# Optimization experiments

Measured on AMD Instinct MI355X. Metric: run time of the kernel, lower is better.

The kernel has to match this reference:

```python
import jax, jax.numpy as jnp
import numpy as np

NEG_INF = -1e30  # stands in for torch's -inf diagonal mask; exp() underflows to 0 identically


def conv1x1(x, w, b):
    # x: [B,C,H,W], w: [O,C], b: [O]
    return jnp.einsum('oc,bchw->bohw', w, x) + b[None, :, None, None]


def s_module(x, qw, qb, kw, kb, vw, vb, gamma):
    # CCNet criss-cross attention with -inf diagonal masking on the H branch.
    B, C, H, W = x.shape
    q = conv1x1(x, qw, qb)  # [B,C8,H,W]
    k = conv1x1(x, kw, kb)  # [B,C8,H,W]
    v = conv1x1(x, vw, vb)  # [B,C,H,W]
    # energy_H[b,h,w,g] = <q[b,:,h,w], k[b,:,g,w]>  (attend along column)
    e_h = jnp.einsum('bchw,bcgw->bhwg', q, k)
    diag_mask = jnp.where(jnp.eye(H, dtype=bool), NEG_INF, 0.0).astype(x.dtype)
    e_h = e_h + diag_mask[None, :, None, :]  # mask h == g
    # energy_W[b,h,w,v] = <q[b,:,h,w], k[b,:,h,v]>  (attend along row)
    e_w = jnp.einsum('bchw,bchv->bhwv', q, k)
    att = jax.nn.softmax(jnp.concatenate([e_h, e_w], axis=-1), axis=-1)  # [B,H,W,H+W]
    a_h, a_w = att[..., :H], att[..., H:]
    out_h = jnp.einsum('bcgw,bhwg->bchw', v, a_h)
    out_w = jnp.einsum('bchv,bhwv->bchw', v, a_w)
    return gamma * (out_h + out_w) + x


def cam_module(x, fb, gamma):
    # channel attention: energy [B,C,C], max-sub trick, softmax, bmm back
    B, C, H, W = x.shape
    f = fb.reshape(B, C, H * W)
    energy = jnp.einsum('bcn,bdn->bcd', f, f)
    energy_new = jnp.max(energy, axis=-1, keepdims=True) - energy
    att = jax.nn.softmax(energy_new, axis=-1)
    out = jnp.einsum('bcd,bdn->bcn', att, f).reshape(B, C, H, W)
    return x + gamma * out


def _forward(x, fb, w_conv, b_conv, bn_g, bn_b,
             xq_w, xq_b, xk_w, xk_b, xv_w, xv_b, x_gamma,
             fq_w, fq_b, fk_w, fk_b, fv_w, fv_b, f_gamma,
             pam_gamma, pam_gamma2, cam_gamma):
    # MaxPool2d(kernel=2, stride=2)
    fbd = jax.lax.reduce_window(fb, -jnp.inf, jax.lax.max,
                                (1, 1, 2, 2), (1, 1, 2, 2), 'VALID')
    # convblock: 1x1 conv + BatchNorm (training-mode batch stats) + ReLU
    y = conv1x1(fbd, w_conv, b_conv)
    mu = jnp.mean(y, axis=(0, 2, 3), keepdims=True)
    var = jnp.var(y, axis=(0, 2, 3), keepdims=True)
    y = (y - mu) * jax.lax.rsqrt(var + 1e-5)
    y = y * bn_g[None, :, None, None] + bn_b[None, :, None, None]
    y = jax.nn.relu(y)
    # FeedbackSpatialAttention (PAM)
    x_att = pam_gamma * s_module(x, xq_w, xq_b, xk_w, xk_b, xv_w, xv_b, x_gamma)
    fb_att = s_module(y, fq_w, fq_b, fk_w, fk_b, fv_w, fv_b, f_gamma)
    pam_out = x + x_att + pam_gamma2 * fb_att
    # CAM on (x, processed fb)
    cam_out = cam_module(x, y, cam_gamma)
    return pam_out + cam_out


def setup_inputs() -> dict:
    key = jax.random.key(0)
    ks = jax.random.split(key, 24)
    B, C, H, W = 4, 64, 128, 128
    C8 = C // 8
    d = {
        'x': jax.random.normal(ks[0], (B, C, H, W), jnp.float32),
        'fb': jax.random.normal(ks[1], (B, C, 2 * H, 2 * W), jnp.float32),
        'w_conv': jax.random.normal(ks[2], (C, C), jnp.float32) * 0.05,
        'b_conv': jax.random.normal(ks[3], (C,), jnp.float32) * 0.02,
        'bn_g': jax.random.uniform(ks[4], (C,), jnp.float32, 0.5, 1.5),
        'bn_b': jax.random.normal(ks[5], (C,), jnp.float32) * 0.02,
        'xq_w': jax.random.normal(ks[6], (C8, C), jnp.float32) * 0.05,
        'xq_b': jax.random.normal(ks[7], (C8,), jnp.float32) * 0.02,
        'xk_w': jax.random.normal(ks[8], (C8, C), jnp.float32) * 0.05,
        'xk_b': jax.random.normal(ks[9], (C8,), jnp.float32) * 0.02,
        'xv_w': jax.random.normal(ks[10], (C, C), jnp.float32) * 0.05,
        'xv_b': jax.random.normal(ks[11], (C,), jnp.float32) * 0.02,
        'x_gamma': jax.random.normal(ks[12], (1,), jnp.float32) * 0.1,
        'fq_w': jax.random.normal(ks[13], (C8, C), jnp.float32) * 0.05,
        'fq_b': jax.random.normal(ks[14], (C8,), jnp.float32) * 0.02,
        'fk_w': jax.random.normal(ks[15], (C8, C), jnp.float32) * 0.05,
        'fk_b': jax.random.normal(ks[16], (C8,), jnp.float32) * 0.02,
        'fv_w': jax.random.normal(ks[17], (C, C), jnp.float32) * 0.05,
        'fv_b': jax.random.normal(ks[18], (C,), jnp.float32) * 0.02,
        'f_gamma': jax.random.normal(ks[19], (1,), jnp.float32) * 0.1,
        'pam_gamma': jax.random.normal(ks[20], (1,), jnp.float32) * 0.1,
        'pam_gamma2': jax.random.normal(ks[21], (1,), jnp.float32) * 0.1,
        'cam_gamma': jax.random.normal(ks[22], (1,), jnp.float32) * 0.1,
    }
    return d


def reference(x, fb, w_conv, b_conv, bn_g, bn_b,
              xq_w, xq_b, xk_w, xk_b, xv_w, xv_b, x_gamma,
              fq_w, fq_b, fk_w, fk_b, fv_w, fv_b, f_gamma,
              pam_gamma, pam_gamma2, cam_gamma):
    return _forward(x, fb, w_conv, b_conv, bn_g, bn_b,
                    xq_w, xq_b, xk_w, xk_b, xv_w, xv_b, x_gamma,
                    fq_w, fq_b, fk_w, fk_b, fv_w, fv_b, f_gamma,
                    pam_gamma, pam_gamma2, cam_gamma)
```

## Files before the change

### kernel.cpp

```cpp
#include <hip/hip_runtime.h>
#include <hip/hip_bf16.h>

#define NP 16384
#define NB 4

typedef __hip_bfloat16 bf16;
typedef unsigned short u16;
typedef unsigned short us8 __attribute__((ext_vector_type(8)));
typedef short ss8 __attribute__((ext_vector_type(8)));
typedef float f32x4 __attribute__((ext_vector_type(4)));
__device__ __forceinline__ float bf2f(const bf16 v) { return __bfloat162float(v); }
__device__ __forceinline__ bf16 f2bf(float v) { return __float2bfloat16(v); }
__device__ __forceinline__ float bfu(u16 h) {
  return __uint_as_float(((unsigned)h) << 16);
}
__device__ __forceinline__ u16 fbu(float v) {
  bf16 b = f2bf(v);
  return *(u16*)&b;
}


__global__ __launch_bounds__(256) void k_pool_conv(
    const float* __restrict__ fb, const float* __restrict__ wconv,
    const float* __restrict__ bconv, bf16* __restrict__ Y) {
  __shared__ float wS[64 * 65], bS[64], Xs[4096];
  int tid = threadIdx.x;
  int b = blockIdx.x >> 8, tile = blockIdx.x & 255;
  int n0 = tile * 64;
  for (int i = tid; i < 4096; i += 256) wS[(i >> 6) * 65 + (i & 63)] = wconv[i];
  if (tid < 64) bS[tid] = bconv[tid];
  for (int i = tid; i < 4096; i += 256) {
    int c = i >> 6, px = i & 63;
    int n = n0 + px, h = n >> 7, w = n & 127;
    size_t fbase = ((size_t)((b * 64 + c) * 256 + 2 * h)) * 256 + 2 * w;
    float2 v01 = *(const float2*)(fb + fbase);
    float2 v23 = *(const float2*)(fb + fbase + 256);
    Xs[i] = fmaxf(fmaxf(v01.x, v01.y), fmaxf(v23.x, v23.y));
  }
  __syncthreads();
  int ty = tid >> 4, tx = tid & 15;
  float acc[4][4];
#pragma unroll
  for (int i = 0; i < 4; ++i) {
    float bv = bS[ty + 16 * i];
#pragma unroll
    for (int j = 0; j < 4; ++j) acc[i][j] = bv;
  }
  for (int c = 0; c < 64; ++c) {
    float xv[4], wv[4];
#pragma unroll
    for (int j = 0; j < 4; ++j) xv[j] = Xs[c * 64 + tx * 4 + j];
#pragma unroll
    for (int i = 0; i < 4; ++i) wv[i] = wS[(ty + 16 * i) * 65 + c];
#pragma unroll
    for (int i = 0; i < 4; ++i)
#pragma unroll
      for (int j = 0; j < 4; ++j) acc[i][j] = fmaf(wv[i], xv[j], acc[i][j]);
  }
#pragma unroll
  for (int i = 0; i < 4; ++i) {
    int ch = ty + 16 * i;
    bf16* yb = Y + (size_t)(b * 64 + ch) * NP + n0 + tx * 4;
#pragma unroll
    for (int j = 0; j < 4; ++j) yb[j] = f2bf(acc[i][j]);
  }
}

__global__ __launch_bounds__(256) void k_stats_p1(const bf16* __restrict__ Y,
                                                  float* __restrict__ PS) {
  int blk = blockIdx.x, tid = threadIdx.x;
  int o = blk >> 3, slab = blk & 7;
  int b = slab >> 1, half = slab & 1;
  const us8* vp =
      (const us8*)(Y + ((size_t)(b * 64 + o)) * NP + half * 8192);
  float s = 0.f, ss = 0.f;
#pragma unroll
  for (int it = 0; it < 4; ++it) {
    us8 v = vp[tid + 256 * it];
#pragma unroll
    for (int e = 0; e < 8; ++e) {
      float f = bfu(v[e]);
      s += f;
      ss = fmaf(f, f, ss);
    }
  }
  for (int off = 32; off > 0; off >>= 1) {
    s += __shfl_down(s, off, 64);
    ss += __shfl_down(ss, off, 64);
  }
  __shared__ float sh[8];
  int wv = tid >> 6, ln = tid & 63;
  if (ln == 0) { sh[wv] = s; sh[4 + wv] = ss; }
  __syncthreads();
  if (tid == 0) {
    PS[blk] = sh[0] + sh[1] + sh[2] + sh[3];
    PS[512 + blk] = sh[4] + sh[5] + sh[6] + sh[7];
  }
}

__global__ __launch_bounds__(64) void k_stats_p2(
    const float* __restrict__ PS, const float* __restrict__ bng,
    const float* __restrict__ bnb, float* __restrict__ SCALE,
    float* __restrict__ SHIFT, const float* xg, const float* fg,
    const float* pg, const float* pg2, const float* cg,
    float* __restrict__ HDR) {
  int o = threadIdx.x;
  float s = 0.f, ss = 0.f;
#pragma unroll
  for (int k = 0; k < 8; ++k) {
    s += PS[o * 8 + k];
    ss += PS[512 + o * 8 + k];
  }
  const float inv = 1.0f / (NB * NP);
  float mu = s * inv;
  float var = ss * inv - mu * mu;
  float r = rsqrtf(var + 1e-5f);
  float sc = r * bng[o];
  SCALE[o] = sc;
  SHIFT[o] = bnb[o] - mu * sc;
  if (o == 0) {
    float vpg = pg[0];
    HDR[1] = vpg * xg[0];
    HDR[2] = pg2[0] * fg[0];
    HDR[3] = 2.0f + vpg;
    HDR[4] = pg2[0];
    HDR[5] = cg[0];
  }
}

__global__ __launch_bounds__(256) void k_conv80x2(
    const float* __restrict__ xin, const bf16* __restrict__ Yin,
    const float* __restrict__ SCALE, const float* __restrict__ SHIFT,
    const float* __restrict__ qw0, const float* __restrict__ qb0,
    const float* __restrict__ kw0, const float* __restrict__ kb0,
    const float* __restrict__ vw0, const float* __restrict__ vb0,
    const float* __restrict__ qw1, const float* __restrict__ qb1,
    const float* __restrict__ kw1, const float* __restrict__ kb1,
    const float* __restrict__ vw1, const float* __restrict__ vb1,
    bf16* __restrict__ QK, bf16* __restrict__ V) {
  __shared__ float wS[80 * 65], bS[80];
  __shared__ u16 Xs[4096];
  int tid = threadIdx.x;
  int m = blockIdx.x >> 10;
  int rest = blockIdx.x & 1023;
  int b = rest >> 8, tile = rest & 255;
  int n0 = tile * 64;
  const float* qw = m ? qw1 : qw0;
  const float* qb = m ? qb1 : qb0;
  const float* kw = m ? kw1 : kw0;
  const float* kb = m ? kb1 : kb0;
  const float* vw = m ? vw1 : vw0;
  const float* vb = m ? vb1 : vb0;
  for (int i = tid; i < 512; i += 256) {
    wS[(i >> 6) * 65 + (i & 63)] = qw[i];
    wS[(8 + (i >> 6)) * 65 + (i & 63)] = kw[i];
  }
  for (int i = tid; i < 4096; i += 256)
    wS[(16 + (i >> 6)) * 65 + (i & 63)] = vw[i];
  if (tid < 8) { bS[tid] = qb[tid]; bS[8 + tid] = kb[tid]; }
  if (tid < 64) bS[16 + tid] = vb[tid];
  for (int i = tid; i < 4096; i += 256) {
    int c = i >> 6, px = i & 63;
    size_t idx = (size_t)(b * 64 + c) * NP + n0 + px;
    float v;
    if (m) {
      v = bf2f(Yin[idx]);
      v = fmaf(v, SCALE[c], SHIFT[c]);
      v = fmaxf(v, 0.f);
    } else {
      v = xin[idx];
    }
    Xs[i] = fbu(v);
  }
  __syncthreads();
  int ty = tid >> 4, tx = tid & 15;
  float acc[5][4];
#pragma unroll
  for (int i = 0; i < 5; ++i) {
    float bv = bS[ty + 16 * i];
#pragma unroll
    for (int j = 0; j < 4; ++j) acc[i][j] = bv;
  }
  for (int c = 0; c < 64; ++c) {
    float xv[4], wv[5];
#pragma unroll
    for (int j = 0; j < 4; ++j) xv[j] = bfu(Xs[c * 64 + tx * 4 + j]);
#pragma unroll
    for (int i = 0; i < 5; ++i) wv[i] = wS[(ty + 16 * i) * 65 + c];
#pragma unroll
    for (int i = 0; i < 5; ++i)
#pragma unroll
      for (int j = 0; j < 4; ++j) acc[i][j] = fmaf(wv[i], xv[j], acc[i][j]);
  }
#pragma unroll
  for (int i = 0; i < 5; ++i) {
    int ch = ty + 16 * i;
    bf16* dst;
    size_t base;
    if (ch < 8) {
      dst = QK; base = (size_t)(((m * 2 + 0) * 4 + b) * 8 + ch) * NP;
    } else if (ch < 16) {
      dst = QK; base = (size_t)(((m * 2 + 1) * 4 + b) * 8 + (ch - 8)) * NP;
    } else {
      dst = V; base = (size_t)((m * 4 + b) * 64 + (ch - 16)) * NP;
    }
#pragma unroll
    for (int j = 0; j < 4; ++j) dst[base + n0 + tx * 4 + j] = f2bf(acc[i][j]);
  }
}

__global__ __launch_bounds__(256) void k_transpose2(
    const u16* __restrict__ inA, u16* __restrict__ outA,
    const u16* __restrict__ inB, u16* __restrict__ outB, int nA) {
  int tileId = blockIdx.x & 15;
  int plane = blockIdx.x >> 4;
  const u16* ip;
  u16* op;
  if (plane < nA) {
    ip = inA + (size_t)plane * NP;
    op = outA + (size_t)plane * NP;
  } else {
    ip = inB + (size_t)(plane - nA) * NP;
    op = outB + (size_t)(plane - nA) * NP;
  }
  int th = tileId >> 2, tw = tileId & 3;
  __shared__ u16 t[32][33];
  int lx = threadIdx.x & 31, ly = threadIdx.x >> 5;
  for (int i = 0; i < 32; i += 8)
    t[ly + i][lx] = ip[(size_t)(th * 32 + ly + i) * 128 + tw * 32 + lx];
  __syncthreads();
  for (int i = 0; i < 32; i += 8)
    op[(size_t)(tw * 32 + ly + i) * 128 + th * 32 + lx] = t[lx][ly + i];
}

__global__ __launch_bounds__(256) void k_qk_stats(
    const bf16* __restrict__ QK, const bf16* __restrict__ QKT,
    float* __restrict__ MW, float* __restrict__ LW,
    float* __restrict__ MH, float* __restrict__ LH) {
  int blk = blockIdx.x;
  int m = blk & 1, mode = (blk >> 1) & 1;
  int bid = blk >> 2;
  int b = bid >> 7, pl = bid & 127;
  const bf16* basep = mode ? QKT : QK;
  const bf16* Qp = basep + (size_t)(((m * 2 + 0) * 4 + b) * 8) * NP;
  const bf16* Kp = basep + (size_t)(((m * 2 + 1) * 4 + b) * 8) * NP;
  float* Mo = (mode ? MH : MW) + (size_t)(m * 4 + b) * NP;
  float* Lo = (mode ? LH : LW) + (size_t)(m * 4 + b) * NP;
  __shared__ float qs[1024], ks[1024], red[256];
  int tid = threadIdx.x;
  for (int i = tid; i < 1024; i += 256) {
    int c = i >> 7, j = i & 127;
    qs[i] = bf2f(Qp[(size_t)c * NP + (size_t)pl * 128 + j]);
    ks[i] = bf2f(Kp[(size_t)c * NP + (size_t)pl * 128 + j]);
  }
  __syncthreads();
  int w = tid & 127, half = tid >> 7;
  float qr[8];
#pragma unroll
  for (int c = 0; c < 8; ++c) qr[c] = qs[c * 128 + w];
  float scr[64];
  float mx = -3.0e38f;
#pragma unroll
  for (int v0 = 0; v0 < 64; ++v0) {
    int v = half * 64 + v0;
    float s = 0.f;
#pragma unroll
    for (int c = 0; c < 8; ++c) s = fmaf(qr[c], ks[c * 128 + v], s);
    if (mode && v == w) s = -1.0e30f;
    scr[v0] = s;
    mx = fmaxf(mx, s);
  }
  red[tid] = mx;
  __syncthreads();
  float mj = fmaxf(red[w], red[128 + w]);
  __syncthreads();
  float l = 0.f;
#pragma unroll
  for (int v0 = 0; v0 < 64; ++v0) l += __expf(scr[v0] - mj);
  red[tid] = l;
  __syncthreads();
  if (half == 0) {
    Mo[(size_t)pl * 128 + w] = mj;
    Lo[(size_t)pl * 128 + w] = red[w] + red[128 + w];
  }
}

__global__ __launch_bounds__(256, 4) void k_av(
    const bf16* __restrict__ QK, const bf16* __restrict__ QKT,
    const bf16* __restrict__ V, const bf16* __restrict__ VT,
    const float* __restrict__ MW, const float* __restrict__ LW,
    const float* __restrict__ MH, const float* __restrict__ LH,
    float* __restrict__ OW, bf16* __restrict__ OHT) {
  int blk = blockIdx.x;
  int m = blk & 1, mode = (blk >> 1) & 1;
  int bid = blk >> 2;
  int b = bid >> 7, h = bid & 127;
  const bf16* qkbase = mode ? QKT : QK;
  const bf16* Qp = qkbase + (size_t)(((m * 2 + 0) * 4 + b) * 8) * NP;
  const bf16* Kp = qkbase + (size_t)(((m * 2 + 1) * 4 + b) * 8) * NP;
  const bf16* Vp = (mode ? VT : V) + (size_t)((m * 4 + b) * 64) * NP;
  __shared__ __align__(16) u16 qT[128 * 8];
  __shared__ __align__(16) u16 kT[128 * 8];
  __shared__ __align__(16) u16 Vs[64 * 136];
  __shared__ float Ml[128], Li[128];
  int tid = threadIdx.x;
  {
    int c = (tid >> 4) & 7, vj = tid & 15;
    const bf16* src = (tid < 128) ? Qp : Kp;
    u16* dst = (tid < 128) ? qT : kT;
    const us8* sp = (const us8*)(src + (size_t)c * NP + (size_t)h * 128);
    us8 sv = sp[vj];
#pragma unroll
    for (int e = 0; e < 8; ++e) {
      int j = vj * 8 + e;
      int p = ((j & 7) << 4) | (j >> 3);
      dst[p * 8 + c] = sv[e];
    }
  }
  for (int i2 = tid; i2 < 1024; i2 += 256) {
    int c = i2 >> 4, vj = i2 & 15;
    const us8* vp = (const us8*)(Vp + (size_t)c * NP + (size_t)h * 128);
    us8 vv = vp[vj];
    *(us8*)&Vs[c * 136 + vj * 8] = vv;
  }
  if (tid < 128) {
    size_t sb = (size_t)(m * 4 + b) * NP;
    const float* Mc = mode ? MH : MW;
    const float* Lc = mode ? LH : LW;
    const float* Ms = mode ? MW : MH;
    const float* Ls = mode ? LW : LH;
    float mc = Mc[sb + (size_t)h * 128 + tid];
    float lc = Lc[sb + (size_t)h * 128 + tid];
    float ms = Ms[sb + (size_t)tid * 128 + h];
    float ls = Ls[sb + (size_t)tid * 128 + h];
    float mm = fmaxf(mc, ms);
    float ll = lc * __expf(mc - mm) + ls * __expf(ms - mm);
    Ml[tid] = mm;
    Li[tid] = 1.0f / ll;
  }
  __syncthreads();
  int lane = tid & 63, wv = tid >> 6;
  int il = lane & 15, gq = lane >> 4;
  float* owBase = OW + (size_t)((m * 4 + b) * 64) * NP + (size_t)h * 128;
  bf16* ohBase = OHT + (size_t)((m * 4 + b) * 64) * NP + (size_t)h * 128;
#pragma unroll
  for (int sub = 0; sub < 2; ++sub) {
    int ib = wv * 32 + sub * 16;
    int i = ib + il;
    float mv = Ml[i], li = Li[i];
    int pi = ((i & 7) << 4) | (i >> 3);
    us8 qv = *(const us8*)&qT[pi * 8];
    float qr[8];
#pragma unroll
    for (int c = 0; c < 8; ++c) qr[c] = bfu(qv[c]);
    ss8 afr[4];
#pragma unroll
    for (int ks = 0; ks < 4; ++ks) {
      ss8 af;
#pragma unroll
      for (int e = 0; e < 8; ++e) {
        int j = ks * 32 + gq * 8 + e;
        int pj = ((j & 7) << 4) | (j >> 3);
        us8 kv = *(const us8*)&kT[pj * 8];
        float s = 0.f;
#pragma unroll
        for (int c = 0; c < 8; ++c) s = fmaf(qr[c], bfu(kv[c]), s);
        float ev = __expf(s - mv) * li;
        if (mode && j == i) ev = 0.f;
        af[e] = (short)fbu(ev);
      }
      afr[ks] = af;
    }
#pragma unroll
    for (int ct = 0; ct < 4; ++ct) {
      f32x4 acc = {0.f, 0.f, 0.f, 0.f};
#pragma unroll
      for (int ks = 0; ks < 4; ++ks) {
        ss8 bv = *(const ss8*)&Vs[(ct * 16 + il) * 136 + ks * 32 + gq * 8];
        acc = __builtin_amdgcn_mfma_f32_16x16x32_bf16(afr[ks], bv, acc, 0, 0, 0);
      }
      int cch = ct * 16 + il;
      int i0 = ib + gq * 4;
      if (mode == 0) {
#pragma unroll
        for (int r = 0; r < 4; ++r)
          owBase[(size_t)cch * NP + (size_t)(i0 + r)] = acc[r];
      } else {
#pragma unroll
        for (int r = 0; r < 4; ++r)
          ohBase[(size_t)cch * NP + (size_t)(i0 + r)] = f2bf(acc[r]);
      }
    }
  }
}

__global__ __launch_bounds__(256) void k_merge2(const bf16* __restrict__ OHT,
                                                float* __restrict__ ACC,
                                                const float* __restrict__ HDR) {
  int tileId = blockIdx.x & 15;
  int plane = blockIdx.x >> 4;
  int th = tileId >> 2, tw = tileId & 3;
  __shared__ float t0[32][33], t1[32][33];
  int lx = threadIdx.x & 31, ly = threadIdx.x >> 5;
  const bf16* ip0 = OHT + (size_t)plane * NP;
  const bf16* ip1 = OHT + (size_t)(256 + plane) * NP;
  for (int i = 0; i < 32; i += 8) {
    size_t idx = (size_t)(th * 32 + ly + i) * 128 + tw * 32 + lx;
    t0[ly + i][lx] = bf2f(ip0[idx]);
    t1[ly + i][lx] = bf2f(ip1[idx]);
  }
  __syncthreads();
  float sc0 = HDR[1], sc1 = HDR[2];
  float* op = ACC + (size_t)plane * NP;
  for (int i = 0; i < 32; i += 8) {
    int h = tw * 32 + ly + i, w = th * 32 + lx;
    op[(size_t)h * 128 + w] = sc0 * t0[lx][ly + i] + sc1 * t1[lx][ly + i];
  }
}

__global__ __launch_bounds__(256) void k_gram(const bf16* __restrict__ Y,
                                              const float* __restrict__ SCALE,
                                              const float* __restrict__ SHIFT,
                                              float* __restrict__ GP) {
  int b = blockIdx.x >> 7, ch = (blockIdx.x >> 2) & 31, t = blockIdx.x & 3;
  int tid = threadIdx.x;
  __shared__ float fs[64 * 129];
  int cg = tid >> 4, dg = tid & 15;
  float acc[4][4];
#pragma unroll
  for (int i = 0; i < 4; ++i)
#pragma unroll
    for (int jx = 0; jx < 4; ++jx) acc[i][jx] = 0.f;
  const bf16* yb = Y + (size_t)b * 64 * NP + ch * 512;
  for (int idx = tid; idx < 8192; idx += 256) {
    int c = idx >> 7, j = idx & 127;
    float v = fmaf(bf2f(yb[(size_t)c * NP + t * 128 + j]), SCALE[c], SHIFT[c]);
    fs[c * 129 + j] = fmaxf(v, 0.f);
  }
  __syncthreads();
  for (int j = 0; j < 128; ++j) {
    float a[4], d[4];
#pragma unroll
    for (int i = 0; i < 4; ++i) a[i] = fs[(cg * 4 + i) * 129 + j];
#pragma unroll
    for (int i = 0; i < 4; ++i) d[i] = fs[(dg * 4 + i) * 129 + j];
#pragma unroll
    for (int i = 0; i < 4; ++i)
#pragma unroll
      for (int jx = 0; jx < 4; ++jx) acc[i][jx] = fmaf(a[i], d[jx], acc[i][jx]);
  }
  float* gp = GP + ((size_t)(b * 128) + ch * 4 + t) * 4096;
#pragma unroll
  for (int i = 0; i < 4; ++i)
#pragma unroll
    for (int jx = 0; jx < 4; ++jx)
      gp[(cg * 4 + i) * 64 + dg * 4 + jx] = acc[i][jx];
}

__global__ __launch_bounds__(256) void k_gram_reduce(const float* __restrict__ GP,
                                                     float* __restrict__ CATT) {
  int b = blockIdx.x >> 4, rg = blockIdx.x & 15;
  int tid = threadIdx.x;
  __shared__ float Es[256];
  int e = rg * 256 + tid;
  float s = 0.f;
  for (int k = 0; k < 128; ++k) s += GP[((size_t)b * 128 + k) * 4096 + e];
  Es[tid] = s;
  __syncthreads();
  int wv = tid >> 6, ln = tid & 63;
  float v = Es[wv * 64 + ln];
  float mn = v;
  for (int off = 32; off; off >>= 1) mn = fminf(mn, __shfl_xor(mn, off, 64));
  float ev = __expf(mn - v);
  float ssum = ev;
  for (int off = 32; off; off >>= 1) ssum += __shfl_xor(ssum, off, 64);
  CATT[((size_t)b * 64 + rg * 4 + wv) * 64 + ln] = ev / ssum;
}

__global__ __launch_bounds__(256) void k_final(
    const float* __restrict__ x, const bf16* __restrict__ Y,
    const float* __restrict__ SCALE, const float* __restrict__ SHIFT,
    const float* __restrict__ CATT, const float* __restrict__ OW,
    const float* __restrict__ HDR, float* __restrict__ OUT) {
  __shared__ float attS[64 * 65], Ys[64 * 65];
  int tid = threadIdx.x;
  int b = blockIdx.x >> 8, tile = blockIdx.x & 255;
  int n0 = tile * 64;
  for (int i = tid; i < 4096; i += 256)
    attS[(i >> 6) * 65 + (i & 63)] = CATT[(size_t)b * 4096 + i];
  for (int i = tid; i < 4096; i += 256) {
    int d = i >> 6, px = i & 63;
    float v = fmaf(bf2f(Y[(size_t)(b * 64 + d) * NP + n0 + px]), SCALE[d], SHIFT[d]);
    Ys[d * 65 + px] = fmaxf(v, 0.f);
  }
  __syncthreads();
  int cg = tid >> 4, pgx = tid & 15;
  int c0 = cg * 4, p0 = pgx * 4;
  float acc[4][4];
#pragma unroll
  for (int i = 0; i < 4; ++i)
#pragma unroll
    for (int j = 0; j < 4; ++j) acc[i][j] = 0.f;
  for (int d = 0; d < 64; ++d) {
    float a[4], yv[4];
#pragma unroll
    for (int i = 0; i < 4; ++i) a[i] = attS[(c0 + i) * 65 + d];
#pragma unroll
    for (int j = 0; j < 4; ++j) yv[j] = Ys[d * 65 + p0 + j];
#pragma unroll
    for (int i = 0; i < 4; ++i)
#pragma unroll
      for (int j = 0; j < 4; ++j) acc[i][j] = fmaf(a[i], yv[j], acc[i][j]);
  }
  float c2pg = HDR[3], fpg2 = HDR[4], fcg = HDR[5];
  float sc0 = HDR[1], sc1 = HDR[2];
#pragma unroll
  for (int i = 0; i < 4; ++i) {
    size_t base = (size_t)(b * 64 + c0 + i) * NP + n0 + p0;
    const float* ow0 = OW + base;
    const float* ow1 = OW + (size_t)256 * NP + base;
#pragma unroll
    for (int j = 0; j < 4; ++j) {
      float yv = Ys[(c0 + i) * 65 + p0 + j];
      OUT[base + j] = c2pg * x[base + j] + fpg2 * yv + OUT[base + j] +
                      fcg * acc[i][j] + sc0 * ow0[j] + sc1 * ow1[j];
    }
  }
}

extern "C" void kernel_launch(void* const* d_in, const int* in_sizes, int n_in,
                              void* d_out, int out_size, void* d_ws, size_t ws_size,
                              hipStream_t stream) {
  const float* x = (const float*)d_in[0];
  const float* fbp = (const float*)d_in[1];

  char* base = (char*)d_ws;
  float* HDR = (float*)base;
  float* SCALE = HDR + 16;
  float* SHIFT = SCALE + 64;
  char* p = base + 4096;
  bf16* Y = (bf16*)p;    p += 8388608;
  bf16* QK = (bf16*)p;   p += 4194304;
  bf16* QKT = (bf16*)p;  p += 4194304;
  bf16* V = (bf16*)p;    p += 16777216;
  bf16* VT = (bf16*)p;   p += 16777216;
  float* MW = (float*)p; p += 524288;
  float* LW = (float*)p; p += 524288;
  float* MH = (float*)p; p += 524288;
  float* LH = (float*)p; p += 524288;
  bf16* OHT = (bf16*)p;  p += 16777216;
  float* OW = (float*)p; p += 33554432;
  float* GP = (float*)p; p += 8388608;
  float* CATT = (float*)p; p += 1048576;
  float* ACC = (float*)d_out;
  float* PS = (float*)QK;

  k_pool_conv<<<1024, 256, 0, stream>>>(fbp, (const float*)d_in[2],
                                        (const float*)d_in[3], Y);
  k_stats_p1<<<512, 256, 0, stream>>>(Y, PS);
  k_stats_p2<<<1, 64, 0, stream>>>(PS, (const float*)d_in[4],
                                   (const float*)d_in[5], SCALE, SHIFT,
                                   (const float*)d_in[12], (const float*)d_in[19],
                                   (const float*)d_in[20], (const float*)d_in[21],
                                   (const float*)d_in[22], HDR);

  k_conv80x2<<<2048, 256, 0, stream>>>(
      x, Y, SCALE, SHIFT,
      (const float*)d_in[6], (const float*)d_in[7], (const float*)d_in[8],
      (const float*)d_in[9], (const float*)d_in[10], (const float*)d_in[11],
      (const float*)d_in[13], (const float*)d_in[14], (const float*)d_in[15],
      (const float*)d_in[16], (const float*)d_in[17], (const float*)d_in[18],
      QK, V);
  k_transpose2<<<10240, 256, 0, stream>>>((const u16*)QK, (u16*)QKT,
                                          (const u16*)V, (u16*)VT, 128);
  k_qk_stats<<<2048, 256, 0, stream>>>(QK, QKT, MW, LW, MH, LH);
  k_av<<<2048, 256, 0, stream>>>(QK, QKT, V, VT, MW, LW, MH, LH, OW, OHT);
  k_merge2<<<4096, 256, 0, stream>>>(OHT, ACC, HDR);

  k_gram<<<512, 256, 0, stream>>>(Y, SCALE, SHIFT, GP);
  k_gram_reduce<<<64, 256, 0, stream>>>(GP, CATT);
  k_final<<<1024, 256, 0, stream>>>(x, Y, SCALE, SHIFT, CATT, OW, HDR,
                                    (float*)d_out);
}
```

Baseline: 311.6 us.

## Fuse softmax stats into attention kernel and merge partial outputs flash-style

```diff
diff --git a/kernel.cpp b/kernel.cpp
--- a/kernel.cpp
+++ b/kernel.cpp
@@ -233,63 +233,11 @@
     op[(size_t)(tw * 32 + ly + i) * 128 + th * 32 + lx] = t[lx][ly + i];
 }
 
-__global__ __launch_bounds__(256) void k_qk_stats(
-    const bf16* __restrict__ QK, const bf16* __restrict__ QKT,
-    float* __restrict__ MW, float* __restrict__ LW,
-    float* __restrict__ MH, float* __restrict__ LH) {
-  int blk = blockIdx.x;
-  int m = blk & 1, mode = (blk >> 1) & 1;
-  int bid = blk >> 2;
-  int b = bid >> 7, pl = bid & 127;
-  const bf16* basep = mode ? QKT : QK;
-  const bf16* Qp = basep + (size_t)(((m * 2 + 0) * 4 + b) * 8) * NP;
-  const bf16* Kp = basep + (size_t)(((m * 2 + 1) * 4 + b) * 8) * NP;
-  float* Mo = (mode ? MH : MW) + (size_t)(m * 4 + b) * NP;
-  float* Lo = (mode ? LH : LW) + (size_t)(m * 4 + b) * NP;
-  __shared__ float qs[1024], ks[1024], red[256];
-  int tid = threadIdx.x;
-  for (int i = tid; i < 1024; i += 256) {
-    int c = i >> 7, j = i & 127;
-    qs[i] = bf2f(Qp[(size_t)c * NP + (size_t)pl * 128 + j]);
-    ks[i] = bf2f(Kp[(size_t)c * NP + (size_t)pl * 128 + j]);
-  }
-  __syncthreads();
-  int w = tid & 127, half = tid >> 7;
-  float qr[8];
-#pragma unroll
-  for (int c = 0; c < 8; ++c) qr[c] = qs[c * 128 + w];
-  float scr[64];
-  float mx = -3.0e38f;
-#pragma unroll
-  for (int v0 = 0; v0 < 64; ++v0) {
-    int v = half * 64 + v0;
-    float s = 0.f;
-#pragma unroll
-    for (int c = 0; c < 8; ++c) s = fmaf(qr[c], ks[c * 128 + v], s);
-    if (mode && v == w) s = -1.0e30f;
-    scr[v0] = s;
-    mx = fmaxf(mx, s);
-  }
-  red[tid] = mx;
-  __syncthreads();
-  float mj = fmaxf(red[w], red[128 + w]);
-  __syncthreads();
-  float l = 0.f;
-#pragma unroll
-  for (int v0 = 0; v0 < 64; ++v0) l += __expf(scr[v0] - mj);
-  red[tid] = l;
-  __syncthreads();
-  if (half == 0) {
-    Mo[(size_t)pl * 128 + w] = mj;
-    Lo[(size_t)pl * 128 + w] = red[w] + red[128 + w];
-  }
-}
-
 __global__ __launch_bounds__(256, 4) void k_av(
     const bf16* __restrict__ QK, const bf16* __restrict__ QKT,
     const bf16* __restrict__ V, const bf16* __restrict__ VT,
-    const float* __restrict__ MW, const float* __restrict__ LW,
-    const float* __restrict__ MH, const float* __restrict__ LH,
+    float* __restrict__ MWp, float* __restrict__ LWp,
+    float* __restrict__ MHp, float* __restrict__ LHp,
     float* __restrict__ OW, bf16* __restrict__ OHT) {
   int blk = blockIdx.x;
   int m = blk & 1, mode = (blk >> 1) & 1;
@@ -302,7 +250,6 @@
   __shared__ __align__(16) u16 qT[128 * 8];
   __shared__ __align__(16) u16 kT[128 * 8];
   __shared__ __align__(16) u16 Vs[64 * 136];
-  __shared__ float Ml[128], Li[128];
   int tid = threadIdx.x;
   {
     int c = (tid >> 4) & 7, vj = tid & 15;
@@ -323,40 +270,25 @@
     us8 vv = vp[vj];
     *(us8*)&Vs[c * 136 + vj * 8] = vv;
   }
-  if (tid < 128) {
-    size_t sb = (size_t)(m * 4 + b) * NP;
-    const float* Mc = mode ? MH : MW;
-    const float* Lc = mode ? LH : LW;
-    const float* Ms = mode ? MW : MH;
-    const float* Ls = mode ? LW : LH;
-    float mc = Mc[sb + (size_t)h * 128 + tid];
-    float lc = Lc[sb + (size_t)h * 128 + tid];
-    float ms = Ms[sb + (size_t)tid * 128 + h];
-    float ls = Ls[sb + (size_t)tid * 128 + h];
-    float mm = fmaxf(mc, ms);
-    float ll = lc * __expf(mc - mm) + ls * __expf(ms - mm);
-    Ml[tid] = mm;
-    Li[tid] = 1.0f / ll;
-  }
   __syncthreads();
   int lane = tid & 63, wv = tid >> 6;
   int il = lane & 15, gq = lane >> 4;
+  size_t sb = (size_t)(m * 4 + b) * NP;
   float* owBase = OW + (size_t)((m * 4 + b) * 64) * NP + (size_t)h * 128;
   bf16* ohBase = OHT + (size_t)((m * 4 + b) * 64) * NP + (size_t)h * 128;
 #pragma unroll
   for (int sub = 0; sub < 2; ++sub) {
     int ib = wv * 32 + sub * 16;
     int i = ib + il;
-    float mv = Ml[i], li = Li[i];
     int pi = ((i & 7) << 4) | (i >> 3);
     us8 qv = *(const us8*)&qT[pi * 8];
     float qr[8];
 #pragma unroll
     for (int c = 0; c < 8; ++c) qr[c] = bfu(qv[c]);
-    ss8 afr[4];
+    float scr[4][8];
+    float mrow = -3.0e38f;
 #pragma unroll
     for (int ks = 0; ks < 4; ++ks) {
-      ss8 af;
 #pragma unroll
       for (int e = 0; e < 8; ++e) {
         int j = ks * 32 + gq * 8 + e;
@@ -365,11 +297,36 @@
         float s = 0.f;
 #pragma unroll
         for (int c = 0; c < 8; ++c) s = fmaf(qr[c], bfu(kv[c]), s);
-        float ev = __expf(s - mv) * li;
-        if (mode && j == i) ev = 0.f;
+        if (mode && j == i) s = -1.0e30f;
+        scr[ks][e] = s;
+        mrow = fmaxf(mrow, s);
+      }
+    }
+    mrow = fmaxf(mrow, __shfl_xor(mrow, 16, 64));
+    mrow = fmaxf(mrow, __shfl_xor(mrow, 32, 64));
+    float l = 0.f;
+    ss8 afr[4];
+#pragma unroll
+    for (int ks = 0; ks < 4; ++ks) {
+      ss8 af;
+#pragma unroll
+      for (int e = 0; e < 8; ++e) {
+        float ev = __expf(scr[ks][e] - mrow);
+        l += ev;
         af[e] = (short)fbu(ev);
       }
       afr[ks] = af;
+    }
+    l += __shfl_xor(l, 16, 64);
+    l += __shfl_xor(l, 32, 64);
+    if (gq == 0) {
+      if (mode == 0) {
+        MWp[sb + (size_t)h * 128 + i] = mrow;
+        LWp[sb + (size_t)h * 128 + i] = l;
+      } else {
+        MHp[sb + (size_t)i * 128 + h] = mrow;
+        LHp[sb + (size_t)i * 128 + h] = l;
+      }
     }
 #pragma unroll
     for (int ct = 0; ct < 4; ++ct) {
@@ -394,11 +351,14 @@
   }
 }
 
-__global__ __launch_bounds__(256) void k_merge2(const bf16* __restrict__ OHT,
-                                                float* __restrict__ ACC,
-                                                const float* __restrict__ HDR) {
+__global__ __launch_bounds__(256) void k_merge2(
+    const bf16* __restrict__ OHT, const float* __restrict__ OW,
+    const float* __restrict__ MWp, const float* __restrict__ LWp,
+    const float* __restrict__ MHp, const float* __restrict__ LHp,
+    const float* __restrict__ HDR, float* __restrict__ ACC) {
   int tileId = blockIdx.x & 15;
   int plane = blockIdx.x >> 4;
+  int b = plane >> 6;
   int th = tileId >> 2, tw = tileId & 3;
   __shared__ float t0[32][33], t1[32][33];
   int lx = threadIdx.x & 31, ly = threadIdx.x >> 5;
@@ -412,9 +372,23 @@
   __syncthreads();
   float sc0 = HDR[1], sc1 = HDR[2];
   float* op = ACC + (size_t)plane * NP;
+  const float* ow0 = OW + (size_t)plane * NP;
+  const float* ow1 = OW + (size_t)(256 + plane) * NP;
+  size_t s0 = (size_t)b * NP, s1 = (size_t)(4 + b) * NP;
   for (int i = 0; i < 32; i += 8) {
-    int h = tw * 32 + ly + i, w = th * 32 + lx;
-    op[(size_t)h * 128 + w] = sc0 * t0[lx][ly + i] + sc1 * t1[lx][ly + i];
+    int hh = tw * 32 + ly + i, ww = th * 32 + lx;
+    size_t idx = (size_t)hh * 128 + ww;
+    float mw0 = MWp[s0 + idx], mh0 = MHp[s0 + idx];
+    float M0 = fmaxf(mw0, mh0);
+    float ea0 = __expf(mw0 - M0), eb0 = __expf(mh0 - M0);
+    float inv0 = 1.0f / (LWp[s0 + idx] * ea0 + LHp[s0 + idx] * eb0);
+    float v0 = (ea0 * ow0[idx] + eb0 * t0[lx][ly + i]) * inv0;
+    float mw1 = MWp[s1 + idx], mh1 = MHp[s1 + idx];
+    float M1 = fmaxf(mw1, mh1);
+    float ea1 = __expf(mw1 - M1), eb1 = __expf(mh1 - M1);
+    float inv1 = 1.0f / (LWp[s1 + idx] * ea1 + LHp[s1 + idx] * eb1);
+    float v1 = (ea1 * ow1[idx] + eb1 * t1[lx][ly + i]) * inv1;
+    op[idx] = sc0 * v0 + sc1 * v1;
   }
 }
 
@@ -480,8 +454,8 @@
 __global__ __launch_bounds__(256) void k_final(
     const float* __restrict__ x, const bf16* __restrict__ Y,
     const float* __restrict__ SCALE, const float* __restrict__ SHIFT,
-    const float* __restrict__ CATT, const float* __restrict__ OW,
-    const float* __restrict__ HDR, float* __restrict__ OUT) {
+    const float* __restrict__ CATT, const float* __restrict__ HDR,
+    float* __restrict__ OUT) {
   __shared__ float attS[64 * 65], Ys[64 * 65];
   int tid = threadIdx.x;
   int b = blockIdx.x >> 8, tile = blockIdx.x & 255;
@@ -513,17 +487,14 @@
       for (int j = 0; j < 4; ++j) acc[i][j] = fmaf(a[i], yv[j], acc[i][j]);
   }
   float c2pg = HDR[3], fpg2 = HDR[4], fcg = HDR[5];
-  float sc0 = HDR[1], sc1 = HDR[2];
 #pragma unroll
   for (int i = 0; i < 4; ++i) {
     size_t base = (size_t)(b * 64 + c0 + i) * NP + n0 + p0;
-    const float* ow0 = OW + base;
-    const float* ow1 = OW + (size_t)256 * NP + base;
 #pragma unroll
     for (int j = 0; j < 4; ++j) {
       float yv = Ys[(c0 + i) * 65 + p0 + j];
-      OUT[base + j] = c2pg * x[base + j] + fpg2 * yv + OUT[base + j] +
-                      fcg * acc[i][j] + sc0 * ow0[j] + sc1 * ow1[j];
+      OUT[base + j] =
+          c2pg * x[base + j] + fpg2 * yv + OUT[base + j] + fcg * acc[i][j];
     }
   }
 }
@@ -544,10 +515,10 @@
   bf16* QKT = (bf16*)p;  p += 4194304;
   bf16* V = (bf16*)p;    p += 16777216;
   bf16* VT = (bf16*)p;   p += 16777216;
-  float* MW = (float*)p; p += 524288;
-  float* LW = (float*)p; p += 524288;
-  float* MH = (float*)p; p += 524288;
-  float* LH = (float*)p; p += 524288;
+  float* MWp = (float*)p; p += 524288;
+  float* LWp = (float*)p; p += 524288;
+  float* MHp = (float*)p; p += 524288;
+  float* LHp = (float*)p; p += 524288;
   bf16* OHT = (bf16*)p;  p += 16777216;
   float* OW = (float*)p; p += 33554432;
   float* GP = (float*)p; p += 8388608;
@@ -573,12 +544,11 @@
       QK, V);
   k_transpose2<<<10240, 256, 0, stream>>>((const u16*)QK, (u16*)QKT,
                                           (const u16*)V, (u16*)VT, 128);
-  k_qk_stats<<<2048, 256, 0, stream>>>(QK, QKT, MW, LW, MH, LH);
-  k_av<<<2048, 256, 0, stream>>>(QK, QKT, V, VT, MW, LW, MH, LH, OW, OHT);
-  k_merge2<<<4096, 256, 0, stream>>>(OHT, ACC, HDR);
+  k_av<<<2048, 256, 0, stream>>>(QK, QKT, V, VT, MWp, LWp, MHp, LHp, OW, OHT);
+  k_merge2<<<4096, 256, 0, stream>>>(OHT, OW, MWp, LWp, MHp, LHp, HDR, ACC);
 
   k_gram<<<512, 256, 0, stream>>>(Y, SCALE, SHIFT, GP);
   k_gram_reduce<<<64, 256, 0, stream>>>(GP, CATT);
-  k_final<<<1024, 256, 0, stream>>>(x, Y, SCALE, SHIFT, CATT, OW, HDR,
+  k_final<<<1024, 256, 0, stream>>>(x, Y, SCALE, SHIFT, CATT, HDR,
                                     (float*)d_out);
 }
```

Measured after the change: 301.3 us. 3.3% less time.
